# Kernel optimization log

Hardware: AMD Instinct MI355X
Metric: run time of the kernel (lower is better)

## Reference

```python
import jax, jax.numpy as jnp
import numpy as np

D, H, L, NTYPES, NREL, T2V = 128, 4, 3, 5, 8, 9
NB, NBV, NLT, NC, NT = 50000, 100000, 10000, 2000, 115
EV, ER, NVOTE = 400000, 50000, 100000


def setup_inputs() -> dict:
    key = jax.random.key(0)
    ks = iter(jax.random.split(key, 80))

    def nrm(shape, scale=1.0):
        return jax.random.normal(next(ks), shape, jnp.float32) * scale

    def zeros(*s):
        return jnp.zeros(s, jnp.float32)

    def rint(shape, hi):
        return jax.random.randint(next(ks), shape, 0, hi)

    def runi(n):
        return jax.random.uniform(next(ks), (n,), jnp.float32) * 10.0

    inp = dict(
        x_bill=nrm((NB, 770)), x_bv=nrm((NBV, 390)), x_lt=nrm((NLT, 4)), x_comm=nrm((NC, 65)),
        pb_W=nrm((770, D), 770 ** -0.5), pb_b=zeros(D),
        pbv_W=nrm((390, D), 390 ** -0.5), pbv_b=zeros(D),
        plt_W1=nrm((4, 64), 0.5), plt_b1=zeros(64), plt_W2=nrm((64, D), 0.125), plt_b2=zeros(D),
        pc_W1=nrm((65, D), 65 ** -0.5), pc_b1=zeros(D), pc_W2=nrm((D, D), D ** -0.5), pc_b2=zeros(D),
        topic_emb=nrm((NT, D), 0.1),
        t2v_w0=nrm((1,)), t2v_b0=zeros(1), t2v_wk=nrm((8,)), t2v_bk=zeros(8),
        edge_W=nrm((NREL, T2V, D), T2V ** -0.5), edge_b=zeros(NREL, D),
        sage_Wl=nrm((L, NREL, D, D), D ** -0.5), sage_bl=zeros(L, NREL, D),
        sage_Wr=nrm((L, NREL, D, D), D ** -0.5), sage_br=zeros(L, NREL, D),
        ln_g=jnp.ones((L, NTYPES, D), jnp.float32), ln_b=zeros(L, NTYPES, D),
        xq_W=nrm((D, D), D ** -0.5), xq_b=zeros(D), xk_W=nrm((D, D), D ** -0.5), xk_b=zeros(D),
        xv_W=nrm((D, D), D ** -0.5), xv_b=zeros(D), xo_W=nrm((D, D), D ** -0.5), xo_b=zeros(D),
        v_W1=nrm((4 * D, 2 * D), (4 * D) ** -0.5), v_b1=zeros(2 * D),
        v_W2=nrm((2 * D, D), (2 * D) ** -0.5), v_b2=zeros(D),
        v_Wo=nrm((D, 3), D ** -0.5), v_bo=zeros(3),
        t_isv=runi(NBV), t_vote=runi(EV), t_rev=runi(ER), t_about=runi(NB),
    )
    # edge indices: row0 = src node ids, row1 = dst node ids
    inp['ei_isv'] = jnp.stack([jnp.arange(NBV, dtype=jnp.int32), rint((NBV,), NB)])  # bill_version -> bill
    inp['ei_vote'] = jnp.stack([rint((EV,), NLT), rint((EV,), NBV)])                 # legislator_term -> bill_version
    inp['ei_rev'] = jnp.stack([rint((ER,), NC), rint((ER,), NB)])                    # committee -> bill
    inp['ei_about'] = jnp.stack([jnp.arange(NB, dtype=jnp.int32), rint((NB,), NT)])  # bill -> topic
    inp['t_for_bill'] = rint((NB,), NT)
    inp['vote_lt'] = rint((NVOTE,), NLT)
    inp['vote_bv'] = rint((NVOTE,), NBV)
    return inp


def _t2v(t, w0, b0, wk, bk):
    t1 = t[:, None]
    return jnp.concatenate([t1 * w0 + b0, jnp.sin(t1 * wk + bk)], -1)  # [E, 1+k]


def _ln(x, g, b):
    m = x.mean(-1, keepdims=True)
    v = jnp.mean((x - m) ** 2, -1, keepdims=True)
    return (x - m) * jax.lax.rsqrt(v + 1e-5) * g + b


def _seg_mean(msg, dst, n):
    agg = jax.ops.segment_sum(msg, dst, num_segments=n)
    cnt = jax.ops.segment_sum(jnp.ones((msg.shape[0],), msg.dtype), dst, num_segments=n)
    return agg / jnp.maximum(cnt, 1.0)[:, None]


def reference(x_bill, x_bv, x_lt, x_comm, pb_W, pb_b, pbv_W, pbv_b, plt_W1, plt_b1, plt_W2, plt_b2, pc_W1, pc_b1, pc_W2, pc_b2, topic_emb, t2v_w0, t2v_b0, t2v_wk, t2v_bk, edge_W, edge_b, sage_Wl, sage_bl, sage_Wr, sage_br, ln_g, ln_b, xq_W, xq_b, xk_W, xk_b, xv_W, xv_b, xo_W, xo_b, v_W1, v_b1, v_W2, v_b2, v_Wo, v_bo, t_isv, t_vote, t_rev, t_about, ei_isv, ei_vote, ei_rev, ei_about, t_for_bill, vote_lt, vote_bv):
    # node type index: 0=bill 1=bill_version 2=legislator_term 3=committee 4=topic
    h = [
        x_bill @ pb_W + pb_b,
        x_bv @ pbv_W + pbv_b,
        jax.nn.relu(x_lt @ plt_W1 + plt_b1) @ plt_W2 + plt_b2,
        jax.nn.relu(x_comm @ pc_W1 + pc_b1) @ pc_W2 + pc_b2,
        topic_emb,
    ]
    sizes = [x.shape[0] for x in h]
    # 8 relations: 4 base + ToUndirected reverses (reverse shares edge times, own edge-MLP)
    rels = [
        (1, 0, ei_isv[0], ei_isv[1], t_isv),
        (0, 1, ei_isv[1], ei_isv[0], t_isv),
        (2, 1, ei_vote[0], ei_vote[1], t_vote),
        (1, 2, ei_vote[1], ei_vote[0], t_vote),
        (3, 0, ei_rev[0], ei_rev[1], t_rev),
        (0, 3, ei_rev[1], ei_rev[0], t_rev),
        (0, 4, ei_about[0], ei_about[1], t_about),
        (4, 0, ei_about[1], ei_about[0], t_about),
    ]
    # per-relation edge features: Time2Vec -> Linear(9, d)  (computed once, reused by all layers)
    efeat = [_t2v(r[4], t2v_w0, t2v_b0, t2v_wk, t2v_bk) @ edge_W[i] + edge_b[i] for i, r in enumerate(rels)]
    for l in range(L):
        new = [jnp.zeros_like(x) for x in h]
        for r, (s, d, si, di, _) in enumerate(rels):
            # SAGEConv: mean-aggregate (src features + edge feat), plus root term; relations summed per dst type
            mean = _seg_mean(h[s][si] + efeat[r], di, sizes[d])
            new[d] = new[d] + (mean @ sage_Wl[l, r] + sage_bl[l, r]) + (h[d] @ sage_Wr[l, r] + sage_br[l, r])
        h = [_ln(new[nt], ln_g[l, nt], ln_b[l, nt]) for nt in range(NTYPES)]
    # attentive_version_pool: mean of bill_version embeddings per bill (count + 1e-6 as in source)
    agg = jax.ops.segment_sum(h[1][ei_isv[0]], ei_isv[1], num_segments=sizes[0])
    cnt = jax.ops.segment_sum(jnp.ones((ei_isv.shape[1],), jnp.float32), ei_isv[1], num_segments=sizes[0]) + 1e-6
    h_bill = 0.5 * h[0] + 0.5 * (agg / cnt[:, None])
    # vote head
    b = ei_isv[1][vote_bv]
    t = t_for_bill[b]
    hlt = h[2][vote_lt]
    hbv = h[1][vote_bv]
    htop = h[4][t]
    hb = h_bill[b]
    dk = D // H
    Q = (hlt @ xq_W + xq_b).reshape(-1, H, dk)
    K = (hb @ xk_W + xk_b).reshape(-1, H, dk)
    V = (hb @ xv_W + xv_b).reshape(-1, H, dk)
    a = jax.nn.softmax(jnp.sum(Q * K, -1) / np.sqrt(float(dk)), axis=-1)  # softmax over heads
    ctxt = (a[..., None] * V).reshape(-1, D) @ xo_W + xo_b
    z = jnp.concatenate([hlt, hbv, htop, ctxt], -1)  # [NVOTE, 4d]
    z = jax.nn.relu(z @ v_W1 + v_b1) @ v_W2 + v_b2
    return z @ v_Wo + v_bo  # [NVOTE, 3]
```

## Files before the change

kernel.cpp:

```cpp
#include <hip/hip_runtime.h>
#include <math.h>

constexpr int cNB = 50000, cNBV = 100000, cNLT = 10000, cNC = 2000, cNT = 115;
constexpr int cEV = 400000, cER = 50000, cNVOTE = 100000;
constexpr int cNTOT = cNB + cNBV + cNLT + cNC + cNT;
constexpr int cLAYERS = 3;
constexpr int F9TOT = 362115;
constexpr int ETOT  = 1200000;
constexpr int LS = 40;

typedef __attribute__((ext_vector_type(8))) short bf16x8;
typedef __attribute__((ext_vector_type(4))) float f32x4;

__device__ __forceinline__ ushort f2b(float f) {
  union { float f; uint u; } v; v.f = f;
  uint r = v.u + 0x7fffu + ((v.u >> 16) & 1u);
  return (ushort)(r >> 16);
}
__device__ __forceinline__ float b2f(ushort b) {
  union { uint u; float f; } v; v.u = ((uint)b) << 16; return v.f;
}

struct SageG {
  const ushort* A[5][4];
  const ushort* Wt[5];
  const float* bias[5];
  ushort* C[5];
  int M[5];
  int Ktot[5];
  int blkStart[6];
};

__global__ __launch_bounds__(256)
void gemm_sage(SageG sg)
{
  __shared__ ushort As[2][128 * LS];
  __shared__ ushort Bs[2][128 * LS];
  const int bid = blockIdx.x;
  int t = 0;
  while (bid >= sg.blkStart[t + 1]) ++t;
  const int row0 = (bid - sg.blkStart[t]) << 7;
  const int M = sg.M[t], Ktot = sg.Ktot[t];
  const ushort* Wt = sg.Wt[t];
  const int tid = threadIdx.x;
  const int l = tid & 63, wid = tid >> 6;
  const int wr = wid >> 1, wc = wid & 1;
  const int lr = l & 15, lkh = l >> 4;
  const int srow = tid >> 2, sq = tid & 3;

  f32x4 acc[4][4];
#pragma unroll
  for (int m = 0; m < 4; ++m)
#pragma unroll
    for (int n = 0; n < 4; ++n) acc[m][n] = (f32x4)0.f;

  uint4 pa0, pa1, pb0, pb1;
  auto loadAB = [&](int kk) {
    const ushort* Ap = sg.A[t][kk >> 7];
    const int k0 = kk & 127;
    {
      const int gr = row0 + srow;
      pa0 = make_uint4(0, 0, 0, 0);
      if (gr < M) pa0 = *(const uint4*)(Ap + (size_t)gr * 128 + k0 + sq * 8);
      pb0 = *(const uint4*)(Wt + (size_t)srow * Ktot + kk + sq * 8);
    }
    {
      const int gr = row0 + srow + 64;
      pa1 = make_uint4(0, 0, 0, 0);
      if (gr < M) pa1 = *(const uint4*)(Ap + (size_t)gr * 128 + k0 + sq * 8);
      pb1 = *(const uint4*)(Wt + (size_t)(srow + 64) * Ktot + kk + sq * 8);
    }
  };
  auto storeLDS = [&](int b) {
    *(uint4*)&As[b][srow * LS + sq * 8] = pa0;
    *(uint4*)&As[b][(srow + 64) * LS + sq * 8] = pa1;
    *(uint4*)&Bs[b][srow * LS + sq * 8] = pb0;
    *(uint4*)&Bs[b][(srow + 64) * LS + sq * 8] = pb1;
  };

  loadAB(0);
  storeLDS(0);
  if (32 < Ktot) loadAB(32);
  __syncthreads();
  int cur = 0;
  for (int kk = 0; kk < Ktot; kk += 32) {
    if (kk + 32 < Ktot) {
      storeLDS(cur ^ 1);
      if (kk + 64 < Ktot) loadAB(kk + 64);
    }
    bf16x8 af[4], bf[4];
#pragma unroll
    for (int m = 0; m < 4; ++m)
      af[m] = *(const bf16x8*)&As[cur][(wr * 64 + m * 16 + lr) * LS + lkh * 8];
#pragma unroll
    for (int n = 0; n < 4; ++n)
      bf[n] = *(const bf16x8*)&Bs[cur][(wc * 64 + n * 16 + lr) * LS + lkh * 8];
#pragma unroll
    for (int m = 0; m < 4; ++m)
#pragma unroll
      for (int n = 0; n < 4; ++n)
        acc[m][n] = __builtin_amdgcn_mfma_f32_16x16x32_bf16(af[m], bf[n], acc[m][n], 0, 0, 0);
    __syncthreads();
    cur ^= 1;
  }

  const float* bias = sg.bias[t];
  ushort* C = sg.C[t];
#pragma unroll
  for (int n = 0; n < 4; ++n) {
    const int col = wc * 64 + n * 16 + lr;
    const float bi = bias[col];
#pragma unroll
    for (int m = 0; m < 4; ++m) {
      const f32x4 v = acc[m][n];
      const int rbase = row0 + wr * 64 + m * 16 + lkh * 4;
#pragma unroll
      for (int j = 0; j < 4; ++j) {
        const int gr = rbase + j;
        if (gr < M) C[(size_t)gr * 128 + col] = f2b(v[j] + bi);
      }
    }
  }
}

template<int NSEG, bool RELU>
__global__ __launch_bounds__(256)
void gemm_abf(const ushort* __restrict__ A0, const ushort* __restrict__ A1,
              const ushort* __restrict__ A2, const ushort* __restrict__ A3,
              int Astride, const ushort* __restrict__ Wt, int Ktot,
              const float* __restrict__ bias, ushort* __restrict__ C,
              int Cstride, int M)
{
  __shared__ ushort As[2][128 * LS];
  __shared__ ushort Bs[2][128 * LS];
  const int tid = threadIdx.x;
  const int row0 = blockIdx.y << 7;
  const int col0 = blockIdx.x << 7;
  const int l = tid & 63, wid = tid >> 6;
  const int wr = wid >> 1, wc = wid & 1;
  const int lr = l & 15, lkh = l >> 4;
  const int srow = tid >> 2, sq = tid & 3;

  f32x4 acc[4][4];
#pragma unroll
  for (int m = 0; m < 4; ++m)
#pragma unroll
    for (int n = 0; n < 4; ++n) acc[m][n] = (f32x4)0.f;

  const int KT2 = NSEG * 128;
  uint4 pa0, pa1, pb0, pb1;
  auto loadAB = [&](int kk) {
    const int ks = kk >> 7;
    const ushort* Ap = (ks == 0) ? A0 : (ks == 1) ? A1 : (ks == 2) ? A2 : A3;
    const int k0 = kk & 127;
    {
      const int gr = row0 + srow;
      pa0 = make_uint4(0, 0, 0, 0);
      if (gr < M) pa0 = *(const uint4*)(Ap + (size_t)gr * Astride + k0 + sq * 8);
      pb0 = *(const uint4*)(Wt + (size_t)(col0 + srow) * Ktot + kk + sq * 8);
    }
    {
      const int gr = row0 + srow + 64;
      pa1 = make_uint4(0, 0, 0, 0);
      if (gr < M) pa1 = *(const uint4*)(Ap + (size_t)gr * Astride + k0 + sq * 8);
      pb1 = *(const uint4*)(Wt + (size_t)(col0 + srow + 64) * Ktot + kk + sq * 8);
    }
  };
  auto storeLDS = [&](int b) {
    *(uint4*)&As[b][srow * LS + sq * 8] = pa0;
    *(uint4*)&As[b][(srow + 64) * LS + sq * 8] = pa1;
    *(uint4*)&Bs[b][srow * LS + sq * 8] = pb0;
    *(uint4*)&Bs[b][(srow + 64) * LS + sq * 8] = pb1;
  };

  loadAB(0);
  storeLDS(0);
  if (32 < KT2) loadAB(32);
  __syncthreads();
  int cur = 0;
  for (int kk = 0; kk < KT2; kk += 32) {
    if (kk + 32 < KT2) {
      storeLDS(cur ^ 1);
      if (kk + 64 < KT2) loadAB(kk + 64);
    }
    bf16x8 af[4], bf[4];
#pragma unroll
    for (int m = 0; m < 4; ++m)
      af[m] = *(const bf16x8*)&As[cur][(wr * 64 + m * 16 + lr) * LS + lkh * 8];
#pragma unroll
    for (int n = 0; n < 4; ++n)
      bf[n] = *(const bf16x8*)&Bs[cur][(wc * 64 + n * 16 + lr) * LS + lkh * 8];
#pragma unroll
    for (int m = 0; m < 4; ++m)
#pragma unroll
      for (int n = 0; n < 4; ++n)
        acc[m][n] = __builtin_amdgcn_mfma_f32_16x16x32_bf16(af[m], bf[n], acc[m][n], 0, 0, 0);
    __syncthreads();
    cur ^= 1;
  }

#pragma unroll
  for (int n = 0; n < 4; ++n) {
    const int col = col0 + wc * 64 + n * 16 + lr;
    const float bi = bias[col];
#pragma unroll
    for (int m = 0; m < 4; ++m) {
      const f32x4 v = acc[m][n];
      const int rbase = row0 + wr * 64 + m * 16 + lkh * 4;
#pragma unroll
      for (int j = 0; j < 4; ++j) {
        const int gr = rbase + j;
        if (gr < M) {
          float x = v[j] + bi;
          if (RELU) x = fmaxf(x, 0.f);
          C[(size_t)gr * Cstride + col] = f2b(x);
        }
      }
    }
  }
}

template<bool RELU>
__global__ __launch_bounds__(256)
void gemm_gat4(const ushort* __restrict__ A0, const int* __restrict__ i0,
               const ushort* __restrict__ A1, const int* __restrict__ i1,
               const ushort* __restrict__ A2, const int* __restrict__ i2,
               const ushort* __restrict__ A3,
               const ushort* __restrict__ Wt, const float* __restrict__ bias,
               ushort* __restrict__ C, int Cstride, int M)
{
  __shared__ ushort As[2][128 * LS];
  __shared__ ushort Bs[2][128 * LS];
  const int tid = threadIdx.x;
  const int row0 = blockIdx.y << 7;
  const int col0 = blockIdx.x << 7;
  const int l = tid & 63, wid = tid >> 6;
  const int wr = wid >> 1, wc = wid & 1;
  const int lr = l & 15, lkh = l >> 4;
  const int srow = tid >> 2, sq = tid & 3;

  f32x4 acc[4][4];
#pragma unroll
  for (int m = 0; m < 4; ++m)
#pragma unroll
    for (int n = 0; n < 4; ++n) acc[m][n] = (f32x4)0.f;

  uint4 pa0, pa1, pb0, pb1;
  auto loadAB = [&](int kk) {
    const int ks = kk >> 7;
    const ushort* Ap = (ks == 0) ? A0 : (ks == 1) ? A1 : (ks == 2) ? A2 : A3;
    const int* ip = (ks == 0) ? i0 : (ks == 1) ? i1 : (ks == 2) ? i2 : nullptr;
    const int k0 = kk & 127;
    {
      const int gr = row0 + srow;
      pa0 = make_uint4(0, 0, 0, 0);
      if (gr < M) {
        const int ar = ip ? ip[gr] : gr;
        pa0 = *(const uint4*)(Ap + (size_t)ar * 128 + k0 + sq * 8);
      }
      pb0 = *(const uint4*)(Wt + (size_t)(col0 + srow) * 512 + kk + sq * 8);
    }
    {
      const int gr = row0 + srow + 64;
      pa1 = make_uint4(0, 0, 0, 0);
      if (gr < M) {
        const int ar = ip ? ip[gr] : gr;
        pa1 = *(const uint4*)(Ap + (size_t)ar * 128 + k0 + sq * 8);
      }
      pb1 = *(const uint4*)(Wt + (size_t)(col0 + srow + 64) * 512 + kk + sq * 8);
    }
  };
  auto storeLDS = [&](int b) {
    *(uint4*)&As[b][srow * LS + sq * 8] = pa0;
    *(uint4*)&As[b][(srow + 64) * LS + sq * 8] = pa1;
    *(uint4*)&Bs[b][srow * LS + sq * 8] = pb0;
    *(uint4*)&Bs[b][(srow + 64) * LS + sq * 8] = pb1;
  };

  loadAB(0);
  storeLDS(0);
  loadAB(32);
  __syncthreads();
  int cur = 0;
  for (int kk = 0; kk < 512; kk += 32) {
    if (kk + 32 < 512) {
      storeLDS(cur ^ 1);
      if (kk + 64 < 512) loadAB(kk + 64);
    }
    bf16x8 af[4], bf[4];
#pragma unroll
    for (int m = 0; m < 4; ++m)
      af[m] = *(const bf16x8*)&As[cur][(wr * 64 + m * 16 + lr) * LS + lkh * 8];
#pragma unroll
    for (int n = 0; n < 4; ++n)
      bf[n] = *(const bf16x8*)&Bs[cur][(wc * 64 + n * 16 + lr) * LS + lkh * 8];
#pragma unroll
    for (int m = 0; m < 4; ++m)
#pragma unroll
      for (int n = 0; n < 4; ++n)
        acc[m][n] = __builtin_amdgcn_mfma_f32_16x16x32_bf16(af[m], bf[n], acc[m][n], 0, 0, 0);
    __syncthreads();
    cur ^= 1;
  }

#pragma unroll
  for (int n = 0; n < 4; ++n) {
    const int col = col0 + wc * 64 + n * 16 + lr;
    const float bi = bias[col];
#pragma unroll
    for (int m = 0; m < 4; ++m) {
      const f32x4 v = acc[m][n];
      const int rbase = row0 + wr * 64 + m * 16 + lkh * 4;
#pragma unroll
      for (int j = 0; j < 4; ++j) {
        const int gr = rbase + j;
        if (gr < M) {
          float x = v[j] + bi;
          if (RELU) x = fmaxf(x, 0.f);
          C[(size_t)gr * Cstride + col] = f2b(x);
        }
      }
    }
  }
}

struct ProjG {
  const float* A[2];
  int Kin[2], Kp[2];
  const ushort* Wt[2];
  const float* bias[2];
  ushort* C[2];
  int M[2];
  int blkStart[3];
};

__global__ __launch_bounds__(256)
void gemm_proj(ProjG pg)
{
  __shared__ ushort As[2][128 * LS];
  __shared__ ushort Bs[2][128 * LS];
  const int bid = blockIdx.x;
  const int t = (bid >= pg.blkStart[1]) ? 1 : 0;
  const int row0 = (bid - pg.blkStart[t]) << 7;
  const float* A = pg.A[t];
  const ushort* Wt = pg.Wt[t];
  const int Kin = pg.Kin[t], Kp = pg.Kp[t], M = pg.M[t];
  const int tid = threadIdx.x;
  const int l = tid & 63, wid = tid >> 6;
  const int wr = wid >> 1, wc = wid & 1;
  const int lr = l & 15, lkh = l >> 4;
  const int srow = tid >> 2, sq = tid & 3;

  f32x4 acc[4][4];
#pragma unroll
  for (int m = 0; m < 4; ++m)
#pragma unroll
    for (int n = 0; n < 4; ++n) acc[m][n] = (f32x4)0.f;

  float4 pfa0, pfa1, pfb0, pfb1;
  uint4 pw0, pw1;
  auto loadP = [&](int kk) {
    const int gk = kk + sq * 8;
    {
      const int gr = row0 + srow;
      float4 f0 = make_float4(0.f, 0.f, 0.f, 0.f), f1 = f0;
      if (gr < M) {
        const float* ap = A + (size_t)gr * Kin + gk;
        if (gk + 7 < Kin) { f0 = *(const float4*)ap; f1 = *(const float4*)(ap + 4); }
        else {
          float tv[8];
#pragma unroll
          for (int j = 0; j < 8; ++j) tv[j] = (gk + j < Kin) ? ap[j] : 0.f;
          f0 = make_float4(tv[0], tv[1], tv[2], tv[3]);
          f1 = make_float4(tv[4], tv[5], tv[6], tv[7]);
        }
      }
      pfa0 = f0; pfa1 = f1;
      pw0 = *(const uint4*)(Wt + (size_t)srow * Kp + kk + sq * 8);
    }
    {
      const int gr = row0 + srow + 64;
      float4 f0 = make_float4(0.f, 0.f, 0.f, 0.f), f1 = f0;
      if (gr < M) {
        const float* ap = A + (size_t)gr * Kin + gk;
        if (gk + 7 < Kin) { f0 = *(const float4*)ap; f1 = *(const float4*)(ap + 4); }
        else {
          float tv[8];
#pragma unroll
          for (int j = 0; j < 8; ++j) tv[j] = (gk + j < Kin) ? ap[j] : 0.f;
          f0 = make_float4(tv[0], tv[1], tv[2], tv[3]);
          f1 = make_float4(tv[4], tv[5], tv[6], tv[7]);
        }
      }
      pfb0 = f0; pfb1 = f1;
      pw1 = *(const uint4*)(Wt + (size_t)(srow + 64) * Kp + kk + sq * 8);
    }
  };
  auto storeP = [&](int b) {
    uint4 w;
    w.x = f2b(pfa0.x) | ((uint)f2b(pfa0.y) << 16);
    w.y = f2b(pfa0.z) | ((uint)f2b(pfa0.w) << 16);
    w.z = f2b(pfa1.x) | ((uint)f2b(pfa1.y) << 16);
    w.w = f2b(pfa1.z) | ((uint)f2b(pfa1.w) << 16);
    *(uint4*)&As[b][srow * LS + sq * 8] = w;
    uint4 v;
    v.x = f2b(pfb0.x) | ((uint)f2b(pfb0.y) << 16);
    v.y = f2b(pfb0.z) | ((uint)f2b(pfb0.w) << 16);
    v.z = f2b(pfb1.x) | ((uint)f2b(pfb1.y) << 16);
    v.w = f2b(pfb1.z) | ((uint)f2b(pfb1.w) << 16);
    *(uint4*)&As[b][(srow + 64) * LS + sq * 8] = v;
    *(uint4*)&Bs[b][srow * LS + sq * 8] = pw0;
    *(uint4*)&Bs[b][(srow + 64) * LS + sq * 8] = pw1;
  };

  loadP(0);
  storeP(0);
  if (32 < Kp) loadP(32);
  __syncthreads();
  int cur = 0;
  for (int kk = 0; kk < Kp; kk += 32) {
    if (kk + 32 < Kp) {
      storeP(cur ^ 1);
      if (kk + 64 < Kp) loadP(kk + 64);
    }
    bf16x8 af[4], bf[4];
#pragma unroll
    for (int m = 0; m < 4; ++m)
      af[m] = *(const bf16x8*)&As[cur][(wr * 64 + m * 16 + lr) * LS + lkh * 8];
#pragma unroll
    for (int n = 0; n < 4; ++n)
      bf[n] = *(const bf16x8*)&Bs[cur][(wc * 64 + n * 16 + lr) * LS + lkh * 8];
#pragma unroll
    for (int m = 0; m < 4; ++m)
#pragma unroll
      for (int n = 0; n < 4; ++n)
        acc[m][n] = __builtin_amdgcn_mfma_f32_16x16x32_bf16(af[m], bf[n], acc[m][n], 0, 0, 0);
    __syncthreads();
    cur ^= 1;
  }

  const float* bias = pg.bias[t];
  ushort* C = pg.C[t];
#pragma unroll
  for (int n = 0; n < 4; ++n) {
    const int col = wc * 64 + n * 16 + lr;
    const float bi = bias[col];
#pragma unroll
    for (int m = 0; m < 4; ++m) {
      const f32x4 v = acc[m][n];
      const int rbase = row0 + wr * 64 + m * 16 + lkh * 4;
#pragma unroll
      for (int j = 0; j < 4; ++j) {
        const int gr = rbase + j;
        if (gr < M) C[(size_t)gr * 128 + col] = f2b(v[j] + bi);
      }
    }
  }
}

__global__ void conv_wt(const float* __restrict__ W, ushort* __restrict__ Wt,
                        int K, int N, int Kp)
{
  const int kp = blockIdx.x * 256 + threadIdx.x;
  const int n = blockIdx.y;
  if (kp >= Kp) return;
  const float v = (kp < K) ? W[(size_t)kp * N + n] : 0.f;
  Wt[(size_t)n * Kp + kp] = f2b(v);
}

__global__ void conv_wcat(const float* __restrict__ Wl, const float* __restrict__ bl,
                          const float* __restrict__ Wr, const float* __restrict__ br,
                          ushort* __restrict__ WC, float* __restrict__ BC)
{
  const int KT[5]   = {512, 384, 256, 256, 256};
  const int TOFF[5] = {0, 512 * 128, 896 * 128, 1152 * 128, 1408 * 128};
  const int RL[5][3] = {{0, 4, 7}, {1, 2, -1}, {3, -1, -1}, {5, -1, -1}, {6, -1, -1}};
  const int NS[5] = {3, 2, 1, 1, 1};
  const int lt = blockIdx.y;
  const int lay = lt / 5, tt = lt % 5;
  const int idx = blockIdx.x * 256 + threadIdx.x;
  const int kk = idx >> 7, n = idx & 127;
  const int Kt = KT[tt];
  ushort* w = WC + (size_t)lay * (1664 * 128) + TOFF[tt] + (size_t)n * Kt;
  float s = 0.f;
  for (int q = 0; q < NS[tt]; ++q) {
    const int r = RL[tt][q];
    s += Wr[((size_t)lay * 8 + r) * 16384 + kk * 128 + n];
    w[(q + 1) * 128 + kk] = f2b(Wl[((size_t)lay * 8 + r) * 16384 + kk * 128 + n]);
  }
  w[kk] = f2b(s);
  if (kk == 0) {
    float b = 0.f;
    for (int q = 0; q < NS[tt]; ++q) {
      const int r = RL[tt][q];
      b += bl[(lay * 8 + r) * 128 + n] + br[(lay * 8 + r) * 128 + n];
    }
    BC[lt * 128 + n] = b;
  }
}

__global__ void conv_head(const float* __restrict__ vW1, const float* __restrict__ vb1,
                          const float* __restrict__ xoW, const float* __restrict__ xob,
                          ushort* __restrict__ WH, float* __restrict__ BH)
{
  const int idx = blockIdx.x * 256 + threadIdx.x;
  const int n = idx >> 9, k = idx & 511;
  if (k < 384) {
    WH[(size_t)n * 512 + k] = f2b(vW1[(size_t)k * 256 + n]);
  } else {
    const int c = k - 384;
    float s = 0.f;
    for (int d = 0; d < 128; ++d)
      s += xoW[c * 128 + d] * vW1[(size_t)(384 + d) * 256 + n];
    WH[(size_t)n * 512 + k] = f2b(s);
    if (c == 0) {
      float bb = vb1[n];
      for (int d = 0; d < 128; ++d)
        bb += xob[d] * vW1[(size_t)(384 + d) * 256 + n];
      BH[n] = bb;
    }
  }
}

__global__ void concat_bias2(const float* __restrict__ a, const float* __restrict__ b,
                             float* __restrict__ o)
{
  const int i = threadIdx.x;
  o[i] = (i < 128) ? a[i] : b[i - 128];
}

__global__ void conv_f2b_kernel(const float* __restrict__ in, ushort* __restrict__ out, int n)
{
  const int i = blockIdx.x * 256 + threadIdx.x;
  if (i < n) out[i] = f2b(in[i]);
}

__global__ void proj_lt_kernel(const float* __restrict__ X, const float* __restrict__ W1,
                               const float* __restrict__ b1, const float* __restrict__ W2,
                               const float* __restrict__ b2, ushort* __restrict__ Y, int n)
{
  __shared__ float xs[4];
  __shared__ float hid[64];
  const int node = blockIdx.x, tid = threadIdx.x;
  if (node >= n) return;
  if (tid < 4) xs[tid] = X[(size_t)node * 4 + tid];
  __syncthreads();
  if (tid < 64) {
    float a = b1[tid];
#pragma unroll
    for (int k = 0; k < 4; ++k) a += xs[k] * W1[k * 64 + tid];
    hid[tid] = fmaxf(a, 0.f);
  }
  __syncthreads();
  float o = b2[tid];
  for (int k = 0; k < 64; ++k) o += hid[k] * W2[k * 128 + tid];
  Y[(size_t)node * 128 + tid] = f2b(o);
}

__global__ void proj_comm_kernel(const float* __restrict__ X, const float* __restrict__ W1,
                                 const float* __restrict__ b1, const float* __restrict__ W2,
                                 const float* __restrict__ b2, ushort* __restrict__ Y, int n)
{
  __shared__ float xs[65];
  __shared__ float hid[128];
  const int node = blockIdx.x, tid = threadIdx.x;
  if (node >= n) return;
  if (tid < 65) xs[tid] = X[(size_t)node * 65 + tid];
  __syncthreads();
  float a = b1[tid];
  for (int k = 0; k < 65; ++k) a += xs[k] * W1[k * 128 + tid];
  hid[tid] = fmaxf(a, 0.f);
  __syncthreads();
  float o = b2[tid];
  for (int k = 0; k < 128; ++k) o += hid[k] * W2[k * 128 + tid];
  Y[(size_t)node * 128 + tid] = f2b(o);
}

struct EdgesAll {
  const int* src[8];
  const int* dst[8];
  int estart[9];
  int f9off[8];
};

__global__ void hist_all(EdgesAll ea, int* __restrict__ deg)
{
  const int e = blockIdx.x * 256 + threadIdx.x;
  if (e >= ea.estart[8]) return;
  int r = 0;
  while (e >= ea.estart[r + 1]) ++r;
  const int el = e - ea.estart[r];
  atomicAdd(&deg[ea.f9off[r] + ea.dst[r][el]], 1);
}

__global__ void fill_all(EdgesAll ea, const int* __restrict__ rp,
                         int* __restrict__ cur, int2* __restrict__ col)
{
  const int e = blockIdx.x * 256 + threadIdx.x;
  if (e >= ea.estart[8]) return;
  int r = 0;
  while (e >= ea.estart[r + 1]) ++r;
  const int el = e - ea.estart[r];
  const int d = ea.f9off[r] + ea.dst[r][el];
  const int p = atomicAdd(&cur[d], 1);
  col[rp[d] + p] = make_int2(ea.src[r][el], el);
}

__global__ __launch_bounds__(256)
void scan_blk(const int* __restrict__ in, int* __restrict__ out,
              int* __restrict__ bsum, int n)
{
  __shared__ int wsum[4];
  const int t = threadIdx.x;
  const int base = blockIdx.x * 1024 + t * 4;
  const int v0 = (base + 0 < n) ? in[base + 0] : 0;
  const int v1 = (base + 1 < n) ? in[base + 1] : 0;
  const int v2 = (base + 2 < n) ? in[base + 2] : 0;
  const int v3 = (base + 3 < n) ? in[base + 3] : 0;
  const int s = v0 + v1 + v2 + v3;
  const int lane = t & 63;
  int incl = s;
#pragma unroll
  for (int m = 1; m < 64; m <<= 1) {
    const int o = __shfl_up(incl, m);
    if (lane >= m) incl += o;
  }
  const int wid = t >> 6;
  if (lane == 63) wsum[wid] = incl;
  __syncthreads();
  int woff = 0;
#pragma unroll
  for (int w = 0; w < 3; ++w) woff += (w < wid) ? wsum[w] : 0;
  int run = woff + incl - s;
  if (base + 0 < n) out[base + 0] = run; run += v0;
  if (base + 1 < n) out[base + 1] = run; run += v1;
  if (base + 2 < n) out[base + 2] = run; run += v2;
  if (base + 3 < n) out[base + 3] = run;
  if (bsum != nullptr && t == 255) bsum[blockIdx.x] = woff + incl;
}

__global__ void scan_add(int* __restrict__ rp, const int* __restrict__ bsum, int n)
{
  const int i = blockIdx.x * 1024 + threadIdx.x * 4;
  const int add = bsum[blockIdx.x];
#pragma unroll
  for (int k = 0; k < 4; ++k)
    if (i + k < n) rp[i + k] += add;
}

struct F9All {
  const float* tt[8];
  int f9off[9];
};

__global__ __launch_bounds__(256)
void f9_thread(F9All fa, const int2* __restrict__ col, const int* __restrict__ rp,
               const float* __restrict__ w0p, const float* __restrict__ b0p,
               const float* __restrict__ wkp, const float* __restrict__ bkp,
               float* __restrict__ F9)
{
  const int node = blockIdx.x * 256 + threadIdx.x;
  if (node >= F9TOT) return;
  float* fo = F9 + (size_t)node * 9;
  if (node >= 312000 && node < 312115) {
#pragma unroll
    for (int k = 0; k < 9; ++k) fo[k] = 0.f;
    return;
  }
  int r = 0;
  while (node >= fa.f9off[r + 1]) ++r;
  const float* tvals = fa.tt[r];
  const int e0 = rp[node], e1 = rp[node + 1];
  const float w0 = w0p[0], b0 = b0p[0];
  float wk[8], bk[8];
#pragma unroll
  for (int k = 0; k < 8; ++k) { wk[k] = wkp[k]; bk[k] = bkp[k]; }
  float st = 0.f;
  float fk[8];
#pragma unroll
  for (int k = 0; k < 8; ++k) fk[k] = 0.f;
  for (int e = e0; e < e1; ++e) {
    const float tv = tvals[col[e].y];
    st += tv;
#pragma unroll
    for (int k = 0; k < 8; ++k) fk[k] += __sinf(tv * wk[k] + bk[k]);
  }
  fo[0] = st * w0 + (float)(e1 - e0) * b0;
#pragma unroll
  for (int k = 0; k < 8; ++k) fo[1 + k] = fk[k];
}

__global__ void f9_topic(const int2* __restrict__ col, const int* __restrict__ rp,
                         const float* __restrict__ tvals,
                         const float* __restrict__ w0p, const float* __restrict__ b0p,
                         const float* __restrict__ wkp, const float* __restrict__ bkp,
                         float* __restrict__ F9)
{
  const int t = blockIdx.x * 256 + threadIdx.x;
  if (t >= cNT * 64) return;
  const int node = t >> 6, j = t & 63;
  const int e0 = rp[node], e1 = rp[node + 1];
  const float w0 = w0p[0], b0 = b0p[0];
  float wk[8], bk[8];
#pragma unroll
  for (int k = 0; k < 8; ++k) { wk[k] = wkp[k]; bk[k] = bkp[k]; }
  float st = 0.f;
  float fk[8];
#pragma unroll
  for (int k = 0; k < 8; ++k) fk[k] = 0.f;
  int cnt = 0;
  for (int e = e0 + j; e < e1; e += 64) {
    const float tv = tvals[col[e].y];
    st += tv; ++cnt;
#pragma unroll
    for (int k = 0; k < 8; ++k) fk[k] += __sinf(tv * wk[k] + bk[k]);
  }
  float* fo = F9 + (size_t)node * 9;
  atomicAdd(fo, st * w0 + (float)cnt * b0);
#pragma unroll
  for (int k = 0; k < 8; ++k) atomicAdd(fo + 1 + k, fk[k]);
}

constexpr int QW_SPLIT0 = 312000;
constexpr int QW_SPLIT1 = 312000 + 115 * 64;
constexpr int QW_TOTAL  = QW_SPLIT1 + 50000;

struct GatherAll {
  const ushort* Hsrc[8];
  const float* eW;
  const float* eb;
  const int2* col;
  const int* rp;
  const float* F9;
  ushort* S;
  float* SPtop;
  int f9off[7];
};

__global__ __launch_bounds__(256)
void gather_all(GatherAll ga)
{
  const int qw = (blockIdx.x * 256 + threadIdx.x) >> 4;
  if (qw >= QW_TOTAL) return;
  const int lq = threadIdx.x & 15;
  int node, r, splitj = -1;
  if (qw < QW_SPLIT0) {
    node = qw;
    r = 0;
    while (node >= ga.f9off[r + 1]) ++r;
  } else if (qw < QW_SPLIT1) {
    const int lw = qw - QW_SPLIT0;
    node = QW_SPLIT0 + (lw >> 6);
    splitj = lw & 63;
// ... 453 lines not shown
```

Baseline: 1.359 ms.

## Drop LDS staging in sage and projection GEMMs, load MFMA fragments directly from global

The gemm_sage and gemm_proj kernels no longer stage A and B tiles through double-buffered shared memory with barriers. Each wave now owns a 32-row by 128-column output strip and loads its MFMA fragments straight from global memory. The weight fragments are re-read by every wave and come from the cache, and the fp32-to-bf16 conversion of A is done in registers. This removes LDS traffic and __syncthreads, but loses both the cross-wave reuse of B and the software prefetch that overlapped loads with MFMA work, so the kernels may become latency-bound on global loads.

```diff
diff --git a/kernel.cpp b/kernel.cpp
--- a/kernel.cpp
+++ b/kernel.cpp
@@ -11,6 +11,7 @@
 
 typedef __attribute__((ext_vector_type(8))) short bf16x8;
 typedef __attribute__((ext_vector_type(4))) float f32x4;
+union pack8 { uint4 u; bf16x8 v; };
 
 __device__ __forceinline__ ushort f2b(float f) {
   union { float f; uint u; } v; v.f = f;
@@ -34,8 +35,6 @@
 __global__ __launch_bounds__(256)
 void gemm_sage(SageG sg)
 {
-  __shared__ ushort As[2][128 * LS];
-  __shared__ ushort Bs[2][128 * LS];
   const int bid = blockIdx.x;
   int t = 0;
   while (bid >= sg.blkStart[t + 1]) ++t;
@@ -44,76 +43,48 @@
   const ushort* Wt = sg.Wt[t];
   const int tid = threadIdx.x;
   const int l = tid & 63, wid = tid >> 6;
-  const int wr = wid >> 1, wc = wid & 1;
   const int lr = l & 15, lkh = l >> 4;
-  const int srow = tid >> 2, sq = tid & 3;
-
-  f32x4 acc[4][4];
-#pragma unroll
-  for (int m = 0; m < 4; ++m)
-#pragma unroll
-    for (int n = 0; n < 4; ++n) acc[m][n] = (f32x4)0.f;
-
-  uint4 pa0, pa1, pb0, pb1;
-  auto loadAB = [&](int kk) {
+  const int r0w = row0 + wid * 32;
+
+  f32x4 acc[2][8];
+#pragma unroll
+  for (int m = 0; m < 2; ++m)
+#pragma unroll
+    for (int n = 0; n < 8; ++n) acc[m][n] = (f32x4)0.f;
+
+  for (int kk = 0; kk < Ktot; kk += 32) {
     const ushort* Ap = sg.A[t][kk >> 7];
-    const int k0 = kk & 127;
-    {
-      const int gr = row0 + srow;
-      pa0 = make_uint4(0, 0, 0, 0);
-      if (gr < M) pa0 = *(const uint4*)(Ap + (size_t)gr * 128 + k0 + sq * 8);
-      pb0 = *(const uint4*)(Wt + (size_t)srow * Ktot + kk + sq * 8);
-    }
-    {
-      const int gr = row0 + srow + 64;
-      pa1 = make_uint4(0, 0, 0, 0);
-      if (gr < M) pa1 = *(const uint4*)(Ap + (size_t)gr * 128 + k0 + sq * 8);
-      pb1 = *(const uint4*)(Wt + (size_t)(srow + 64) * Ktot + kk + sq * 8);
-    }
-  };
-  auto storeLDS = [&](int b) {
-    *(uint4*)&As[b][srow * LS + sq * 8] = pa0;
-    *(uint4*)&As[b][(srow + 64) * LS + sq * 8] = pa1;
-    *(uint4*)&Bs[b][srow * LS + sq * 8] = pb0;
-    *(uint4*)&Bs[b][(srow + 64) * LS + sq * 8] = pb1;
-  };
-
-  loadAB(0);
-  storeLDS(0);
-  if (32 < Ktot) loadAB(32);
-  __syncthreads();
-  int cur = 0;
-  for (int kk = 0; kk < Ktot; kk += 32) {
-    if (kk + 32 < Ktot) {
-      storeLDS(cur ^ 1);
-      if (kk + 64 < Ktot) loadAB(kk + 64);
-    }
-    bf16x8 af[4], bf[4];
-#pragma unroll
-    for (int m = 0; m < 4; ++m)
-      af[m] = *(const bf16x8*)&As[cur][(wr * 64 + m * 16 + lr) * LS + lkh * 8];
-#pragma unroll
-    for (int n = 0; n < 4; ++n)
-      bf[n] = *(const bf16x8*)&Bs[cur][(wc * 64 + n * 16 + lr) * LS + lkh * 8];
-#pragma unroll
-    for (int m = 0; m < 4; ++m)
-#pragma unroll
-      for (int n = 0; n < 4; ++n)
+    const int k0 = (kk & 127) + lkh * 8;
+    bf16x8 af[2];
+#pragma unroll
+    for (int m = 0; m < 2; ++m) {
+      const int gr = r0w + m * 16 + lr;
+      pack8 p; p.u = make_uint4(0, 0, 0, 0);
+      if (gr < M) p.u = *(const uint4*)(Ap + (size_t)gr * 128 + k0);
+      af[m] = p.v;
+    }
+    const int gk = kk + lkh * 8;
+    bf16x8 bf[8];
+#pragma unroll
+    for (int n = 0; n < 8; ++n)
+      bf[n] = *(const bf16x8*)(Wt + (size_t)(n * 16 + lr) * Ktot + gk);
+#pragma unroll
+    for (int m = 0; m < 2; ++m)
+#pragma unroll
+      for (int n = 0; n < 8; ++n)
         acc[m][n] = __builtin_amdgcn_mfma_f32_16x16x32_bf16(af[m], bf[n], acc[m][n], 0, 0, 0);
-    __syncthreads();
-    cur ^= 1;
   }
 
   const float* bias = sg.bias[t];
   ushort* C = sg.C[t];
 #pragma unroll
-  for (int n = 0; n < 4; ++n) {
-    const int col = wc * 64 + n * 16 + lr;
+  for (int n = 0; n < 8; ++n) {
+    const int col = n * 16 + lr;
     const float bi = bias[col];
 #pragma unroll
-    for (int m = 0; m < 4; ++m) {
+    for (int m = 0; m < 2; ++m) {
       const f32x4 v = acc[m][n];
-      const int rbase = row0 + wr * 64 + m * 16 + lkh * 4;
+      const int rbase = r0w + m * 16 + lkh * 4;
 #pragma unroll
       for (int j = 0; j < 4; ++j) {
         const int gr = rbase + j;
@@ -337,8 +308,6 @@
 __global__ __launch_bounds__(256)
 void gemm_proj(ProjG pg)
 {
-  __shared__ ushort As[2][128 * LS];
-  __shared__ ushort Bs[2][128 * LS];
   const int bid = blockIdx.x;
   const int t = (bid >= pg.blkStart[1]) ? 1 : 0;
   const int row0 = (bid - pg.blkStart[t]) << 7;
@@ -347,108 +316,64 @@
   const int Kin = pg.Kin[t], Kp = pg.Kp[t], M = pg.M[t];
   const int tid = threadIdx.x;
   const int l = tid & 63, wid = tid >> 6;
-  const int wr = wid >> 1, wc = wid & 1;
   const int lr = l & 15, lkh = l >> 4;
-  const int srow = tid >> 2, sq = tid & 3;
-
-  f32x4 acc[4][4];
-#pragma unroll
-  for (int m = 0; m < 4; ++m)
-#pragma unroll
-    for (int n = 0; n < 4; ++n) acc[m][n] = (f32x4)0.f;
-
-  float4 pfa0, pfa1, pfb0, pfb1;
-  uint4 pw0, pw1;
-  auto loadP = [&](int kk) {
-    const int gk = kk + sq * 8;
-    {
-      const int gr = row0 + srow;
-      float4 f0 = make_float4(0.f, 0.f, 0.f, 0.f), f1 = f0;
+  const int r0w = row0 + wid * 32;
+
+  f32x4 acc[2][8];
+#pragma unroll
+  for (int m = 0; m < 2; ++m)
+#pragma unroll
+    for (int n = 0; n < 8; ++n) acc[m][n] = (f32x4)0.f;
+
+  for (int kk = 0; kk < Kp; kk += 32) {
+    const int gk = kk + lkh * 8;
+    bf16x8 af[2];
+#pragma unroll
+    for (int m = 0; m < 2; ++m) {
+      const int gr = r0w + m * 16 + lr;
+      float f[8];
+#pragma unroll
+      for (int j = 0; j < 8; ++j) f[j] = 0.f;
       if (gr < M) {
         const float* ap = A + (size_t)gr * Kin + gk;
-        if (gk + 7 < Kin) { f0 = *(const float4*)ap; f1 = *(const float4*)(ap + 4); }
-        else {
-          float tv[8];
-#pragma unroll
-          for (int j = 0; j < 8; ++j) tv[j] = (gk + j < Kin) ? ap[j] : 0.f;
-          f0 = make_float4(tv[0], tv[1], tv[2], tv[3]);
-          f1 = make_float4(tv[4], tv[5], tv[6], tv[7]);
+        if (gk + 7 < Kin) {
+          const float4 f0 = *(const float4*)ap;
+          const float4 f1 = *(const float4*)(ap + 4);
+          f[0] = f0.x; f[1] = f0.y; f[2] = f0.z; f[3] = f0.w;
+          f[4] = f1.x; f[5] = f1.y; f[6] = f1.z; f[7] = f1.w;
+        } else {
+#pragma unroll
+          for (int j = 0; j < 8; ++j) f[j] = (gk + j < Kin) ? ap[j] : 0.f;
         }
       }
-      pfa0 = f0; pfa1 = f1;
-      pw0 = *(const uint4*)(Wt + (size_t)srow * Kp + kk + sq * 8);
-    }
-    {
-      const int gr = row0 + srow + 64;
-      float4 f0 = make_float4(0.f, 0.f, 0.f, 0.f), f1 = f0;
-      if (gr < M) {
-        const float* ap = A + (size_t)gr * Kin + gk;
-        if (gk + 7 < Kin) { f0 = *(const float4*)ap; f1 = *(const float4*)(ap + 4); }
-        else {
-          float tv[8];
-#pragma unroll
-          for (int j = 0; j < 8; ++j) tv[j] = (gk + j < Kin) ? ap[j] : 0.f;
-          f0 = make_float4(tv[0], tv[1], tv[2], tv[3]);
-          f1 = make_float4(tv[4], tv[5], tv[6], tv[7]);
-        }
-      }
-      pfb0 = f0; pfb1 = f1;
-      pw1 = *(const uint4*)(Wt + (size_t)(srow + 64) * Kp + kk + sq * 8);
-    }
-  };
-  auto storeP = [&](int b) {
-    uint4 w;
-    w.x = f2b(pfa0.x) | ((uint)f2b(pfa0.y) << 16);
-    w.y = f2b(pfa0.z) | ((uint)f2b(pfa0.w) << 16);
-    w.z = f2b(pfa1.x) | ((uint)f2b(pfa1.y) << 16);
-    w.w = f2b(pfa1.z) | ((uint)f2b(pfa1.w) << 16);
-    *(uint4*)&As[b][srow * LS + sq * 8] = w;
-    uint4 v;
-    v.x = f2b(pfb0.x) | ((uint)f2b(pfb0.y) << 16);
-    v.y = f2b(pfb0.z) | ((uint)f2b(pfb0.w) << 16);
-    v.z = f2b(pfb1.x) | ((uint)f2b(pfb1.y) << 16);
-    v.w = f2b(pfb1.z) | ((uint)f2b(pfb1.w) << 16);
-    *(uint4*)&As[b][(srow + 64) * LS + sq * 8] = v;
-    *(uint4*)&Bs[b][srow * LS + sq * 8] = pw0;
-    *(uint4*)&Bs[b][(srow + 64) * LS + sq * 8] = pw1;
-  };
-
-  loadP(0);
-  storeP(0);
-  if (32 < Kp) loadP(32);
-  __syncthreads();
-  int cur = 0;
-  for (int kk = 0; kk < Kp; kk += 32) {
-    if (kk + 32 < Kp) {
-      storeP(cur ^ 1);
-      if (kk + 64 < Kp) loadP(kk + 64);
-    }
-    bf16x8 af[4], bf[4];
-#pragma unroll
-    for (int m = 0; m < 4; ++m)
-      af[m] = *(const bf16x8*)&As[cur][(wr * 64 + m * 16 + lr) * LS + lkh * 8];
-#pragma unroll
-    for (int n = 0; n < 4; ++n)
-      bf[n] = *(const bf16x8*)&Bs[cur][(wc * 64 + n * 16 + lr) * LS + lkh * 8];
-#pragma unroll
-    for (int m = 0; m < 4; ++m)
-#pragma unroll
-      for (int n = 0; n < 4; ++n)
+      pack8 p;
+      p.u.x = f2b(f[0]) | ((uint)f2b(f[1]) << 16);
+      p.u.y = f2b(f[2]) | ((uint)f2b(f[3]) << 16);
+      p.u.z = f2b(f[4]) | ((uint)f2b(f[5]) << 16);
+      p.u.w = f2b(f[6]) | ((uint)f2b(f[7]) << 16);
+      af[m] = p.v;
+    }
+    bf16x8 bf[8];
+#pragma unroll
+    for (int n = 0; n < 8; ++n)
+      bf[n] = *(const bf16x8*)(Wt + (size_t)(n * 16 + lr) * Kp + gk);
+#pragma unroll
+    for (int m = 0; m < 2; ++m)
+#pragma unroll
+      for (int n = 0; n < 8; ++n)
         acc[m][n] = __builtin_amdgcn_mfma_f32_16x16x32_bf16(af[m], bf[n], acc[m][n], 0, 0, 0);
-    __syncthreads();
-    cur ^= 1;
   }
 
   const float* bias = pg.bias[t];
   ushort* C = pg.C[t];
 #pragma unroll
-  for (int n = 0; n < 4; ++n) {
-    const int col = wc * 64 + n * 16 + lr;
+  for (int n = 0; n < 8; ++n) {
+    const int col = n * 16 + lr;
     const float bi = bias[col];
 #pragma unroll
-    for (int m = 0; m < 4; ++m) {
+    for (int m = 0; m < 2; ++m) {
       const f32x4 v = acc[m][n];
-      const int rbase = row0 + wr * 64 + m * 16 + lkh * 4;
+      const int rbase = r0w + m * 16 + lkh * 4;
 #pragma unroll
       for (int j = 0; j < 4; ++j) {
         const int gr = rbase + j;
```

Result: slower. 1.544 ms (+13.6%).
